# Kernel tuning notes

Measured on AMD Instinct MI355X. Metric: run time of the kernel, lower is better.

The kernel has to match this reference:

```python
import jax, jax.numpy as jnp
import numpy as np

K_NEIGHBORS = 32
TEMP = 0.5

def setup_inputs() -> dict:
    key = jax.random.key(0)
    k1, k2, k3 = jax.random.split(key, 3)
    B, D, N, F = 32, 256, 16384, 256
    query = jax.random.normal(k1, (B, D), dtype=jnp.float32)
    keys = jax.random.normal(k2, (B, D, N), dtype=jnp.float32)
    values = jax.random.normal(k3, (B, F, N), dtype=jnp.float32)
    return {"query": query, "keys": keys, "values": values}

def _compute_omega(s, k, t):
    # s: [..., N] similarities. Returns omega: [..., N, K]
    alpha0 = jax.nn.softmax(s, axis=-1)

    def step(alpha, _):
        om = jax.nn.softmax(alpha / t, axis=-1)
        alpha_new = alpha + jnp.log1p(-om)
        return alpha_new, om

    _, omegas = jax.lax.scan(step, alpha0, None, length=k)  # [K, ..., N]
    return jnp.moveaxis(omegas, 0, -1)  # [..., N, K]

def reference(query, keys, values):
    D = query.shape[-1]
    # sims: [..., N]; note the negative sign from the original module
    sims = -jnp.einsum('...d,...dn->...n', query, keys) / jnp.sqrt(jnp.float32(D))
    omega = _compute_omega(sims, K_NEIGHBORS, TEMP)  # [..., N, K]
    # weighted gather-sum: [..., K, F]
    k_nearest = jnp.einsum('...nk,...fn->...kf', omega, values)
    return k_nearest
```

## Files before the change

### kernel.cpp

```cpp
#include <hip/hip_runtime.h>
#include <hip/hip_bf16.h>

#define B_ 32
#define D_ 256
#define N_ 16384
#define F_ 256
#define K_ 32

#define NSPLIT 16
#define NSLICE (N_ / NSPLIT)

#define L2E 1.4426950408889634f

typedef __attribute__((ext_vector_type(8))) short bf16x8;
typedef __attribute__((ext_vector_type(4))) float f32x4;

__device__ __forceinline__ unsigned short f2bf(float x) {
    unsigned int u = __float_as_uint(x);
    u = (u + 0x7FFFu + ((u >> 16) & 1u)) >> 16;
    return (unsigned short)u;
}

__device__ __forceinline__ unsigned int pack_bf16(float x, float y) {
    unsigned int ux = __float_as_uint(x), uy = __float_as_uint(y);
    ux = (ux + 0x7FFFu + ((ux >> 16) & 1u)) >> 16;
    uy = (uy + 0x7FFFu + ((uy >> 16) & 1u)) & 0xFFFF0000u;
    return ux | uy;
}

__global__ __launch_bounds__(256) void sims_kernel(
    const float* __restrict__ q, const float* __restrict__ keys, float* __restrict__ sims)
{
    const int nt = N_ / 1024;
    int b = blockIdx.x / nt;
    int tile = blockIdx.x % nt;
    int n0 = tile * 1024 + threadIdx.x * 4;

    __shared__ float qs[D_];
    qs[threadIdx.x] = q[b * D_ + threadIdx.x];
    __syncthreads();

    const float* kb = keys + (size_t)b * D_ * N_ + n0;
    float ax = 0.f, ay = 0.f, az = 0.f, aw = 0.f;
    #pragma unroll 4
    for (int d = 0; d < D_; ++d) {
        float4 kv = *reinterpret_cast<const float4*>(kb + (size_t)d * N_);
        float qd = qs[d];
        ax = fmaf(qd, kv.x, ax); ay = fmaf(qd, kv.y, ay);
        az = fmaf(qd, kv.z, az); aw = fmaf(qd, kv.w, aw);
    }
    const float sc = -0.0625f;
    float4 o = make_float4(ax * sc, ay * sc, az * sc, aw * sc);
    *reinterpret_cast<float4*>(sims + b * N_ + n0) = o;
}

__device__ __forceinline__ float blk_max(float v, volatile float* red) {
    #pragma unroll
    for (int off = 32; off > 0; off >>= 1) v = fmaxf(v, __shfl_xor(v, off));
    if ((threadIdx.x & 63) == 0) red[threadIdx.x >> 6] = v;
    __syncthreads();
    if (threadIdx.x < 64) {
        float w = (threadIdx.x < 16) ? red[threadIdx.x] : -3.0e38f;
        #pragma unroll
        for (int off = 8; off > 0; off >>= 1) w = fmaxf(w, __shfl_xor(w, off));
        if (threadIdx.x == 0) red[16] = w;
    }
    __syncthreads();
    return red[16];
}
__device__ __forceinline__ float blk_sum(float v, volatile float* red) {
    #pragma unroll
    for (int off = 32; off > 0; off >>= 1) v += __shfl_xor(v, off);
    if ((threadIdx.x & 63) == 0) red[threadIdx.x >> 6] = v;
    __syncthreads();
    if (threadIdx.x < 64) {
        float w = (threadIdx.x < 16) ? red[threadIdx.x] : 0.0f;
        #pragma unroll
        for (int off = 8; off > 0; off >>= 1) w += __shfl_xor(w, off);
        if (threadIdx.x == 0) red[16] = w;
    }
    __syncthreads();
    return red[16];
}

__global__ __launch_bounds__(1024) void omega_kernel(
    const float* __restrict__ sims, __hip_bfloat16* __restrict__ omega)
{
    int b = blockIdx.x, t = threadIdx.x;
    __shared__ float red1[17];
    __shared__ float red2[17];

    const float* sb = sims + (size_t)b * N_ + t * 16;
    float a[16];
    #pragma unroll
    for (int j = 0; j < 16; j += 4) {
        float4 v = *reinterpret_cast<const float4*>(sb + j);
        a[j] = v.x; a[j + 1] = v.y; a[j + 2] = v.z; a[j + 3] = v.w;
    }
    float m0 = -3.0e38f;
    #pragma unroll
    for (int j = 0; j < 16; ++j) m0 = fmaxf(m0, a[j]);
    m0 = blk_max(m0, red1);

    float zs = 0.f;
    #pragma unroll
    for (int j = 0; j < 16; ++j) {
        a[j] = __builtin_amdgcn_exp2f((a[j] - m0) * L2E);
        zs += a[j];
    }
    float Z = blk_sum(zs, red2);
    float c2 = 2.0f * L2E / Z;
    #pragma unroll
    for (int j = 0; j < 16; ++j) a[j] = __builtin_amdgcn_exp2f(a[j] * c2);

    unsigned int* ob32 = reinterpret_cast<unsigned int*>(omega) + (size_t)b * K_ * (N_ / 2) + t * 8;

    for (int k = 0; k < K_; ++k) {
        float zz = 0.f;
        #pragma unroll
        for (int j = 0; j < 16; ++j) zz += a[j];
        float Zk = blk_sum(zz, red2);
        float izk = 1.0f / Zk;
        unsigned int pk[8];
        #pragma unroll
        for (int j = 0; j < 16; j += 2) {
            float om0 = a[j] * izk;
            float om1 = a[j + 1] * izk;
            pk[j >> 1] = pack_bf16(om0, om1);
            float u0 = 1.0f - om0, u1 = 1.0f - om1;
            a[j]     *= u0 * u0;
            a[j + 1] *= u1 * u1;
        }
        unsigned int* orow = ob32 + (size_t)k * (N_ / 2);
        *reinterpret_cast<uint4*>(orow)     = make_uint4(pk[0], pk[1], pk[2], pk[3]);
        *reinterpret_cast<uint4*>(orow + 4) = make_uint4(pk[4], pk[5], pk[6], pk[7]);
    }
}

__global__ __launch_bounds__(256) void pv_kernel(
    const float* __restrict__ values, const __hip_bfloat16* __restrict__ omega,
    float* __restrict__ part)
{
    int ns = blockIdx.x % NSPLIT;
    int b  = blockIdx.x / NSPLIT;
    int t = threadIdx.x;
    int wv = t >> 6;
    int l  = t & 63;
    int lr = l & 15;
    int lq = l >> 4;
    int fbase = wv * 64;

    const float* vb = values + (size_t)b * F_ * N_;
    const unsigned short* ob = reinterpret_cast<const unsigned short*>(omega) + (size_t)b * K_ * N_;
    int n0 = ns * NSLICE;

    f32x4 acc[4][2];
    #pragma unroll
    for (int ti = 0; ti < 4; ++ti)
        #pragma unroll
        for (int kt = 0; kt < 2; ++kt)
            acc[ti][kt] = (f32x4){0.f, 0.f, 0.f, 0.f};

    const unsigned short* pa = ob + (size_t)lr * N_ + n0 + lq * 8;

    for (int nb = 0; nb < NSLICE; nb += 32) {
        bf16x8 a0 = *reinterpret_cast<const bf16x8*>(pa + nb);
        bf16x8 a1 = *reinterpret_cast<const bf16x8*>(pa + 16 * N_ + nb);
        #pragma unroll
        for (int ti = 0; ti < 4; ++ti) {
            const float* vp = vb + (size_t)(fbase + ti * 16 + lr) * N_ + n0 + nb + lq * 8;
            float4 x0 = *reinterpret_cast<const float4*>(vp);
            float4 x1 = *reinterpret_cast<const float4*>(vp + 4);
            union { unsigned short s[8]; bf16x8 v; } bv;
            bv.s[0] = f2bf(x0.x); bv.s[1] = f2bf(x0.y);
            bv.s[2] = f2bf(x0.z); bv.s[3] = f2bf(x0.w);
            bv.s[4] = f2bf(x1.x); bv.s[5] = f2bf(x1.y);
            bv.s[6] = f2bf(x1.z); bv.s[7] = f2bf(x1.w);
            acc[ti][0] = __builtin_amdgcn_mfma_f32_16x16x32_bf16(a0, bv.v, acc[ti][0], 0, 0, 0);
            acc[ti][1] = __builtin_amdgcn_mfma_f32_16x16x32_bf16(a1, bv.v, acc[ti][1], 0, 0, 0);
        }
    }

    float* pb = part + ((size_t)(b * NSPLIT + ns) * K_) * F_;
    #pragma unroll
    for (int ti = 0; ti < 4; ++ti) {
        int f = fbase + ti * 16 + lr;
        #pragma unroll
        for (int kt = 0; kt < 2; ++kt) {
            #pragma unroll
            for (int r = 0; r < 4; ++r) {
                int k = kt * 16 + lq * 4 + r;
                pb[(size_t)k * F_ + f] = acc[ti][kt][r];
            }
        }
    }
}

__global__ __launch_bounds__(256) void reduce_kernel(
    const float* __restrict__ part, float* __restrict__ out)
{
    int idx = (blockIdx.x * 256 + threadIdx.x) * 4;
    int f = idx % F_;
    int bk = idx / F_;
    int k = bk % K_;
    int b = bk / K_;
    const float* p = part + (((size_t)b * NSPLIT) * K_ + k) * F_ + f;
    float4 s = make_float4(0.f, 0.f, 0.f, 0.f);
    #pragma unroll 4
    for (int ns = 0; ns < NSPLIT; ++ns) {
        float4 v = *reinterpret_cast<const float4*>(p + (size_t)ns * K_ * F_);
        s.x += v.x; s.y += v.y; s.z += v.z; s.w += v.w;
    }
    *reinterpret_cast<float4*>(out + idx) = s;
}

extern "C" void kernel_launch(void* const* d_in, const int* in_sizes, int n_in,
                              void* d_out, int out_size, void* d_ws, size_t ws_size,
                              hipStream_t stream)
{
    const float* q      = (const float*)d_in[0];
    const float* keys   = (const float*)d_in[1];
    const float* values = (const float*)d_in[2];
    float* out = (float*)d_out;

    char* ws = (char*)d_ws;
    float* sims           = (float*)ws;
    __hip_bfloat16* omega = (__hip_bfloat16*)(ws + (size_t)B_ * N_ * 4);
    float* part           = (float*)(ws + (size_t)B_ * N_ * 4
                                        + (size_t)B_ * K_ * N_ * 2);

    sims_kernel  <<<B_ * (N_ / 1024), 256, 0, stream>>>(q, keys, sims);
    omega_kernel <<<B_, 1024, 0, stream>>>(sims, omega);
    pv_kernel    <<<B_ * NSPLIT, 256, 0, stream>>>(values, omega, part);
    reduce_kernel<<<(B_ * K_ * F_) / 1024, 256, 0, stream>>>(part, out);
}
```

Measured before the change: 299.0 us.

## Recompute omega in pv kernel from per-step normalizers instead of materializing it

The omega kernel no longer writes the full K×N bf16 omega tensor. It stores only the initial weights and the per-step inverse normalizers. The pv kernel rebuilds its omega slice in LDS, using a swizzled layout to avoid bank conflicts, and then runs the MFMA loop. This removes the global write and re-read of roughly 32 MB of omega. In exchange it adds per-block recomputation and 64 KB of LDS per block, which may reduce occupancy of pv_kernel.

Measured after the change: 271.5 us. -9.2%, faster.

```diff
diff --git a/kernel.cpp b/kernel.cpp
--- a/kernel.cpp
+++ b/kernel.cpp
@@ -83,8 +83,8 @@
     return red[16];
 }
 
-__global__ __launch_bounds__(1024) void omega_kernel(
-    const float* __restrict__ sims, __hip_bfloat16* __restrict__ omega)
+__global__ __launch_bounds__(1024) void zeta_kernel(
+    const float* __restrict__ sims, float* __restrict__ w0, float* __restrict__ izeta)
 {
     int b = blockIdx.x, t = threadIdx.x;
     __shared__ float red1[17];
@@ -113,7 +113,10 @@
     #pragma unroll
     for (int j = 0; j < 16; ++j) a[j] = __builtin_amdgcn_exp2f(a[j] * c2);
 
-    unsigned int* ob32 = reinterpret_cast<unsigned int*>(omega) + (size_t)b * K_ * (N_ / 2) + t * 8;
+    float* wp = w0 + (size_t)b * N_ + t * 16;
+    #pragma unroll
+    for (int j = 0; j < 16; j += 4)
+        *reinterpret_cast<float4*>(wp + j) = make_float4(a[j], a[j+1], a[j+2], a[j+3]);
 
     for (int k = 0; k < K_; ++k) {
         float zz = 0.f;
@@ -121,29 +124,47 @@
         for (int j = 0; j < 16; ++j) zz += a[j];
         float Zk = blk_sum(zz, red2);
         float izk = 1.0f / Zk;
-        unsigned int pk[8];
-        #pragma unroll
-        for (int j = 0; j < 16; j += 2) {
-            float om0 = a[j] * izk;
-            float om1 = a[j + 1] * izk;
-            pk[j >> 1] = pack_bf16(om0, om1);
-            float u0 = 1.0f - om0, u1 = 1.0f - om1;
-            a[j]     *= u0 * u0;
-            a[j + 1] *= u1 * u1;
-        }
-        unsigned int* orow = ob32 + (size_t)k * (N_ / 2);
-        *reinterpret_cast<uint4*>(orow)     = make_uint4(pk[0], pk[1], pk[2], pk[3]);
-        *reinterpret_cast<uint4*>(orow + 4) = make_uint4(pk[4], pk[5], pk[6], pk[7]);
+        if (t == 0) izeta[b * K_ + k] = izk;
+        #pragma unroll
+        for (int j = 0; j < 16; ++j) {
+            float u = 1.0f - a[j] * izk;
+            a[j] *= u * u;
+        }
     }
 }
 
 __global__ __launch_bounds__(256) void pv_kernel(
-    const float* __restrict__ values, const __hip_bfloat16* __restrict__ omega,
-    float* __restrict__ part)
+    const float* __restrict__ values, const float* __restrict__ w0,
+    const float* __restrict__ izeta, float* __restrict__ part)
 {
     int ns = blockIdx.x % NSPLIT;
     int b  = blockIdx.x / NSPLIT;
     int t = threadIdx.x;
+
+    __shared__ unsigned char om_lds[K_ * 2048];
+
+    int n0 = ns * NSLICE;
+
+    {
+        float4 u4 = *reinterpret_cast<const float4*>(w0 + (size_t)b * N_ + n0 + t * 4);
+        float u[4] = {u4.x, u4.y, u4.z, u4.w};
+        const float* zb = izeta + b * K_;
+        int colbyte = t * 8;
+        #pragma unroll 8
+        for (int k = 0; k < K_; ++k) {
+            float izk = zb[k];
+            float om0 = u[0] * izk, om1 = u[1] * izk;
+            float om2 = u[2] * izk, om3 = u[3] * izk;
+            unsigned int lo = pack_bf16(om0, om1);
+            unsigned int hi = pack_bf16(om2, om3);
+            int addr = (k * 2048 + colbyte) ^ ((k & 7) << 4);
+            *reinterpret_cast<uint2*>(&om_lds[addr]) = make_uint2(lo, hi);
+            float a0 = 1.f - om0, a1 = 1.f - om1, a2 = 1.f - om2, a3 = 1.f - om3;
+            u[0] *= a0 * a0; u[1] *= a1 * a1; u[2] *= a2 * a2; u[3] *= a3 * a3;
+        }
+    }
+    __syncthreads();
+
     int wv = t >> 6;
     int l  = t & 63;
     int lr = l & 15;
@@ -151,8 +172,6 @@
     int fbase = wv * 64;
 
     const float* vb = values + (size_t)b * F_ * N_;
-    const unsigned short* ob = reinterpret_cast<const unsigned short*>(omega) + (size_t)b * K_ * N_;
-    int n0 = ns * NSLICE;
 
     f32x4 acc[4][2];
     #pragma unroll
@@ -161,11 +180,11 @@
         for (int kt = 0; kt < 2; ++kt)
             acc[ti][kt] = (f32x4){0.f, 0.f, 0.f, 0.f};
 
-    const unsigned short* pa = ob + (size_t)lr * N_ + n0 + lq * 8;
-
     for (int nb = 0; nb < NSLICE; nb += 32) {
-        bf16x8 a0 = *reinterpret_cast<const bf16x8*>(pa + nb);
-        bf16x8 a1 = *reinterpret_cast<const bf16x8*>(pa + 16 * N_ + nb);
+        int cb = (nb + lq * 8) * 2;
+        int xr = (lr & 7) << 4;
+        bf16x8 a0 = *reinterpret_cast<const bf16x8*>(&om_lds[(lr * 2048 + cb) ^ xr]);
+        bf16x8 a1 = *reinterpret_cast<const bf16x8*>(&om_lds[((lr + 16) * 2048 + cb) ^ xr]);
         #pragma unroll
         for (int ti = 0; ti < 4; ++ti) {
             const float* vp = vb + (size_t)(fbase + ti * 16 + lr) * N_ + n0 + nb + lq * 8;
@@ -224,13 +243,13 @@
     float* out = (float*)d_out;
 
     char* ws = (char*)d_ws;
-    float* sims           = (float*)ws;
-    __hip_bfloat16* omega = (__hip_bfloat16*)(ws + (size_t)B_ * N_ * 4);
-    float* part           = (float*)(ws + (size_t)B_ * N_ * 4
-                                        + (size_t)B_ * K_ * N_ * 2);
+    float* sims  = (float*)ws;
+    float* w0    = (float*)(ws + (size_t)B_ * N_ * 4);
+    float* izeta = (float*)(ws + (size_t)2 * B_ * N_ * 4);
+    float* part  = (float*)(ws + (size_t)2 * B_ * N_ * 4 + 4096);
 
     sims_kernel  <<<B_ * (N_ / 1024), 256, 0, stream>>>(q, keys, sims);
-    omega_kernel <<<B_, 1024, 0, stream>>>(sims, omega);
-    pv_kernel    <<<B_ * NSPLIT, 256, 0, stream>>>(values, omega, part);
+    zeta_kernel  <<<B_, 1024, 0, stream>>>(sims, w0, izeta);
+    pv_kernel    <<<B_ * NSPLIT, 256, 0, stream>>>(values, w0, izeta, part);
     reduce_kernel<<<(B_ * K_ * F_) / 1024, 256, 0, stream>>>(part, out);
 }
```
